# Performance work log

Measured on AMD Instinct MI355X. Metric: run time of the kernel, lower is better.

Reference implementation:

```python
import jax, jax.numpy as jnp
import numpy as np

KS = 3          # kernel_size
DIL = 1         # dilation
PAD = DIL * (KS - 1) // 2
HEAD_DIM = 64
SCALE = HEAD_DIM ** (-0.5)


def _unfold_patches(x):
    """Emulate nn.Unfold(KS, DIL, PAD, 1): x [B,d,H,W] -> [B,d,KS*KS,H,W] (zero-padded)."""
    B, d, H, W = x.shape
    xp = jnp.pad(x, ((0, 0), (0, 0), (PAD, PAD), (PAD, PAD)))
    # small fixed loop over the KS*KS kernel offsets (9 slices), same patch order as Unfold
    patches = [xp[:, :, i * DIL:i * DIL + H, j * DIL:j * DIL + W]
               for i in range(KS) for j in range(KS)]
    return jnp.stack(patches, axis=2)  # [B, d, KS*KS, H, W]


def setup_inputs() -> dict:
    key = jax.random.key(0)
    kq, kk, kv = jax.random.split(key, 3)
    shape = (32, 64, 64, 64)  # [B, head_dim, H, W]
    return {
        "q": jax.random.normal(kq, shape, dtype=jnp.float32),
        "k": jax.random.normal(kk, shape, dtype=jnp.float32),
        "v": jax.random.normal(kv, shape, dtype=jnp.float32),
    }


def reference(q, k, v):
    # q: [B,d,H,W]; per-pixel attention over the KS*KS dilated neighborhood of k/v
    k_p = _unfold_patches(k)                                   # [B,d,n,H,W], n = KS*KS
    attn = jnp.einsum('bdhw,bdnhw->bnhw', q, k_p) * SCALE      # [B,n,H,W]
    attn = jax.nn.softmax(attn, axis=1)                        # softmax over window (dim=-1 in torch layout)
    v_p = _unfold_patches(v)                                   # [B,d,n,H,W]
    out = jnp.einsum('bnhw,bdnhw->bdhw', attn, v_p)            # [B,d,H,W]
    return out
```

## Files before the change

kernel.cpp:

```cpp
#include <hip/hip_runtime.h>

namespace {
constexpr int Bn = 32, Dn = 64, Hn = 64, Wn = 64;
constexpr int PLANE = Hn * Wn;
constexpr int NW  = 4;
constexpr int DPW = Dn / NW;
constexpr float SCALE = 0.125f;
typedef float f4a __attribute__((ext_vector_type(4), aligned(4)));
}

__global__ __launch_bounds__(256, 4) void dilate_attn_kernel(
    const float* __restrict__ q, const float* __restrict__ k,
    const float* __restrict__ v, float* __restrict__ out)
{
    __shared__ float2 red[NW][9][64];

    const int t  = threadIdx.x;
    const int l  = t & 63;
    const int wv = t >> 6;
    const int ci = l & 31;
    const int lr = l >> 5;
    const int c  = ci * 2;

    const int bid = blockIdx.x;
    const int swz = (bid & 7) * 128 + (bid >> 3);
    const int b      = swz >> 5;
    const int stripe = swz & 31;
    const int hr     = stripe * 2 + lr;

    const int  base = b * Dn * PLANE;
    const bool ci0 = (ci == 0), ci31 = (ci == 31);

    const int cb = ci0 ? 0 : (ci31 ? (c - 2) : (c - 1));

    int  koff[3];
    bool rok[3];
#pragma unroll
    for (int di = 0; di < 3; ++di) {
        const int kr = hr - 1 + di;
        rok[di] = (kr >= 0) && (kr < Hn);
        const int krc = min(max(kr, 0), Hn - 1);
        koff[di] = krc * Wn + cb;
    }
    const int qoff = hr * Wn + c;

    float a0[9], a1[9];
#pragma unroll
    for (int n = 0; n < 9; ++n) { a0[n] = 0.0f; a1[n] = 0.0f; }

    {
        const float* kp = k + base + wv * DPW * PLANE;
        const float* qp = q + base + wv * DPW * PLANE;
#pragma unroll 4
        for (int ds = 0; ds < DPW; ++ds) {
            const f4a r0 = *(const f4a*)(kp + koff[0]);
            const f4a r1 = *(const f4a*)(kp + koff[1]);
            const f4a r2 = *(const f4a*)(kp + koff[2]);
            const float2 qv = *(const float2*)(qp + qoff);
            kp += PLANE; qp += PLANE;
#pragma unroll
            for (int di = 0; di < 3; ++di) {
                const f4a vv = (di == 0) ? r0 : (di == 1) ? r1 : r2;
                const float w0 = ci31 ? vv.y : vv.x;
                const float w1 = ci0 ? vv.x : (ci31 ? vv.z : vv.y);
                const float w2 = ci0 ? vv.y : (ci31 ? vv.w : vv.z);
                const float w3 = ci0 ? vv.z : vv.w;
                a0[di * 3 + 0] = fmaf(qv.x, w0, a0[di * 3 + 0]);
                a0[di * 3 + 1] = fmaf(qv.x, w1, a0[di * 3 + 1]);
                a0[di * 3 + 2] = fmaf(qv.x, w2, a0[di * 3 + 2]);
                a1[di * 3 + 0] = fmaf(qv.y, w1, a1[di * 3 + 0]);
                a1[di * 3 + 1] = fmaf(qv.y, w2, a1[di * 3 + 1]);
                a1[di * 3 + 2] = fmaf(qv.y, w3, a1[di * 3 + 2]);
            }
        }
    }

#pragma unroll
    for (int n = 0; n < 9; ++n) red[wv][n][l] = make_float2(a0[n], a1[n]);
    __syncthreads();
#pragma unroll
    for (int n = 0; n < 9; ++n) {
        float2 s = red[0][n][l];
#pragma unroll
        for (int ow = 1; ow < NW; ++ow) {
            const float2 p = red[ow][n][l];
            s.x += p.x; s.y += p.y;
        }
        a0[n] = s.x; a1[n] = s.y;
    }

#pragma unroll
    for (int di = 0; di < 3; ++di)
#pragma unroll
        for (int dj = 0; dj < 3; ++dj) {
            const int n = di * 3 + dj;
            a0[n] = (rok[di] && (dj != 0 || !ci0))  ? a0[n] : 0.0f;
            a1[n] = (rok[di] && (dj != 2 || !ci31)) ? a1[n] : 0.0f;
        }
#pragma unroll
    for (int n = 0; n < 9; ++n) { a0[n] *= SCALE; a1[n] *= SCALE; }
    float m0 = a0[0], m1 = a1[0];
#pragma unroll
    for (int n = 1; n < 9; ++n) { m0 = fmaxf(m0, a0[n]); m1 = fmaxf(m1, a1[n]); }
    float s0 = 0.0f, s1 = 0.0f;
#pragma unroll
    for (int n = 0; n < 9; ++n) {
        a0[n] = __expf(a0[n] - m0); s0 += a0[n];
        a1[n] = __expf(a1[n] - m1); s1 += a1[n];
    }
    const float i0 = 1.0f / s0, i1 = 1.0f / s1;
#pragma unroll
    for (int n = 0; n < 9; ++n) { a0[n] *= i0; a1[n] *= i1; }

#pragma unroll
    for (int di = 0; di < 3; ++di)
#pragma unroll
        for (int dj = 0; dj < 3; ++dj) {
            const int n = di * 3 + dj;
            a0[n] = (rok[di] && (dj != 0 || !ci0))  ? a0[n] : 0.0f;
            a1[n] = (rok[di] && (dj != 2 || !ci31)) ? a1[n] : 0.0f;
        }

    {
        const float* vp = v + base + wv * DPW * PLANE;
        float*       op = out + base + wv * DPW * PLANE;
#pragma unroll 4
        for (int ds = 0; ds < DPW; ++ds) {
            const f4a r0 = *(const f4a*)(vp + koff[0]);
            const f4a r1 = *(const f4a*)(vp + koff[1]);
            const f4a r2 = *(const f4a*)(vp + koff[2]);
            vp += PLANE;
            float o0 = 0.0f, o1 = 0.0f;
#pragma unroll
            for (int di = 0; di < 3; ++di) {
                const f4a vv = (di == 0) ? r0 : (di == 1) ? r1 : r2;
                const float w0 = ci31 ? vv.y : vv.x;
                const float w1 = ci0 ? vv.x : (ci31 ? vv.z : vv.y);
                const float w2 = ci0 ? vv.y : (ci31 ? vv.w : vv.z);
                const float w3 = ci0 ? vv.z : vv.w;
                o0 = fmaf(a0[di * 3 + 0], w0, o0);
                o0 = fmaf(a0[di * 3 + 1], w1, o0);
                o0 = fmaf(a0[di * 3 + 2], w2, o0);
                o1 = fmaf(a1[di * 3 + 0], w1, o1);
                o1 = fmaf(a1[di * 3 + 1], w2, o1);
                o1 = fmaf(a1[di * 3 + 2], w3, o1);
            }
            *(float2*)(op + qoff) = make_float2(o0, o1);
            op += PLANE;
        }
    }
}

extern "C" void kernel_launch(void* const* d_in, const int* in_sizes, int n_in,
                              void* d_out, int out_size, void* d_ws, size_t ws_size,
                              hipStream_t stream) {
    const float* q = (const float*)d_in[0];
    const float* k = (const float*)d_in[1];
    const float* v = (const float*)d_in[2];
    float* out = (float*)d_out;
    (void)in_sizes; (void)n_in; (void)out_size; (void)d_ws; (void)ws_size;

    const int grid = Bn * 32;
    dilate_attn_kernel<<<grid, 256, 0, stream>>>(q, k, v, out);
}
```

Measured before the change: 30.14 us.

## Split head dim across 8 waves, parallelize reduction, double-buffer loads

Raises the number of waves per block from 4 to 8, so each wave handles 8 channels instead of 16, and launches 512 threads per block. The cross-wave reduction is rewritten so each wave sums one window slot in shared memory, with the last wave also summing the ninth slot, and a second barrier is added. The K and V loops are fully unrolled with explicit two-stage register double-buffering to overlap loads with FMAs. The aim is more memory-level parallelism and shorter per-wave serial loops, at the cost of an extra barrier, larger blocks and higher register pressure under the 512,8 launch bounds.

```diff
diff --git a/kernel.cpp b/kernel.cpp
--- a/kernel.cpp
+++ b/kernel.cpp
@@ -3,13 +3,13 @@
 namespace {
 constexpr int Bn = 32, Dn = 64, Hn = 64, Wn = 64;
 constexpr int PLANE = Hn * Wn;
-constexpr int NW  = 4;
+constexpr int NW  = 8;
 constexpr int DPW = Dn / NW;
 constexpr float SCALE = 0.125f;
 typedef float f4a __attribute__((ext_vector_type(4), aligned(4)));
 }
 
-__global__ __launch_bounds__(256, 4) void dilate_attn_kernel(
+__global__ __launch_bounds__(512, 8) void dilate_attn_kernel(
     const float* __restrict__ q, const float* __restrict__ k,
     const float* __restrict__ v, float* __restrict__ out)
 {
@@ -30,8 +30,7 @@
 
     const int  base = b * Dn * PLANE;
     const bool ci0 = (ci == 0), ci31 = (ci == 31);
-
-    const int cb = ci0 ? 0 : (ci31 ? (c - 2) : (c - 1));
+    const int  cb = ci0 ? 0 : (ci31 ? (c - 2) : (c - 1));
 
     int  koff[3];
     bool rok[3];
@@ -50,14 +49,20 @@
 
     {
         const float* kp = k + base + wv * DPW * PLANE;
-        const float* qp = q + base + wv * DPW * PLANE;
-#pragma unroll 4
-        for (int ds = 0; ds < DPW; ++ds) {
-            const f4a r0 = *(const f4a*)(kp + koff[0]);
-            const f4a r1 = *(const f4a*)(kp + koff[1]);
-            const f4a r2 = *(const f4a*)(kp + koff[2]);
-            const float2 qv = *(const float2*)(qp + qoff);
-            kp += PLANE; qp += PLANE;
+        const float* qp = q + base + wv * DPW * PLANE + qoff;
+
+        f4a x0, x1, x2; float2 xq;
+        f4a y0, y1, y2; float2 yq;
+
+        auto LDK = [&](int ds, f4a& r0, f4a& r1, f4a& r2, float2& qv) {
+            const float* kk = kp + ds * PLANE;
+            r0 = *(const f4a*)(kk + koff[0]);
+            r1 = *(const f4a*)(kk + koff[1]);
+            r2 = *(const f4a*)(kk + koff[2]);
+            qv = *(const float2*)(qp + ds * PLANE);
+        };
+        auto ACC = [&](const f4a& r0, const f4a& r1, const f4a& r2,
+                       const float2& qv) {
 #pragma unroll
             for (int di = 0; di < 3; ++di) {
                 const f4a vv = (di == 0) ? r0 : (di == 1) ? r1 : r2;
@@ -72,20 +77,43 @@
                 a1[di * 3 + 1] = fmaf(qv.y, w2, a1[di * 3 + 1]);
                 a1[di * 3 + 2] = fmaf(qv.y, w3, a1[di * 3 + 2]);
             }
+        };
+
+        LDK(0, x0, x1, x2, xq);
+#pragma unroll
+        for (int ds = 0; ds < DPW; ds += 2) {
+            if (ds + 1 < DPW) LDK(ds + 1, y0, y1, y2, yq);
+            ACC(x0, x1, x2, xq);
+            if (ds + 2 < DPW) LDK(ds + 2, x0, x1, x2, xq);
+            if (ds + 1 < DPW) ACC(y0, y1, y2, yq);
         }
     }
 
 #pragma unroll
     for (int n = 0; n < 9; ++n) red[wv][n][l] = make_float2(a0[n], a1[n]);
     __syncthreads();
+    {
+        float2 s = red[0][wv][l];
+#pragma unroll
+        for (int sw = 1; sw < NW; ++sw) {
+            const float2 p = red[sw][wv][l];
+            s.x += p.x; s.y += p.y;
+        }
+        red[0][wv][l] = s;
+        if (wv == NW - 1) {
+            float2 s8 = red[0][8][l];
+#pragma unroll
+            for (int sw = 1; sw < NW; ++sw) {
+                const float2 p = red[sw][8][l];
+                s8.x += p.x; s8.y += p.y;
+            }
+            red[0][8][l] = s8;
+        }
+    }
+    __syncthreads();
 #pragma unroll
     for (int n = 0; n < 9; ++n) {
-        float2 s = red[0][n][l];
-#pragma unroll
-        for (int ow = 1; ow < NW; ++ow) {
-            const float2 p = red[ow][n][l];
-            s.x += p.x; s.y += p.y;
-        }
+        const float2 s = red[0][n][l];
         a0[n] = s.x; a1[n] = s.y;
     }
 
@@ -123,13 +151,18 @@
 
     {
         const float* vp = v + base + wv * DPW * PLANE;
-        float*       op = out + base + wv * DPW * PLANE;
-#pragma unroll 4
-        for (int ds = 0; ds < DPW; ++ds) {
-            const f4a r0 = *(const f4a*)(vp + koff[0]);
-            const f4a r1 = *(const f4a*)(vp + koff[1]);
-            const f4a r2 = *(const f4a*)(vp + koff[2]);
-            vp += PLANE;
+        float*       op = out + base + wv * DPW * PLANE + qoff;
+
+        f4a x0, x1, x2;
+        f4a y0, y1, y2;
+
+        auto LDV = [&](int ds, f4a& r0, f4a& r1, f4a& r2) {
+            const float* vk = vp + ds * PLANE;
+            r0 = *(const f4a*)(vk + koff[0]);
+            r1 = *(const f4a*)(vk + koff[1]);
+            r2 = *(const f4a*)(vk + koff[2]);
+        };
+        auto PV = [&](int ds, const f4a& r0, const f4a& r1, const f4a& r2) {
             float o0 = 0.0f, o1 = 0.0f;
 #pragma unroll
             for (int di = 0; di < 3; ++di) {
@@ -145,8 +178,16 @@
                 o1 = fmaf(a1[di * 3 + 1], w2, o1);
                 o1 = fmaf(a1[di * 3 + 2], w3, o1);
             }
-            *(float2*)(op + qoff) = make_float2(o0, o1);
-            op += PLANE;
+            *(float2*)(op + ds * PLANE) = make_float2(o0, o1);
+        };
+
+        LDV(0, x0, x1, x2);
+#pragma unroll
+        for (int ds = 0; ds < DPW; ds += 2) {
+            if (ds + 1 < DPW) LDV(ds + 1, y0, y1, y2);
+            PV(ds, x0, x1, x2);
+            if (ds + 2 < DPW) LDV(ds + 2, x0, x1, x2);
+            if (ds + 1 < DPW) PV(ds + 1, y0, y1, y2);
         }
     }
 }
@@ -161,5 +202,5 @@
     (void)in_sizes; (void)n_in; (void)out_size; (void)d_ws; (void)ws_size;
 
     const int grid = Bn * 32;
-    dilate_attn_kernel<<<grid, 256, 0, stream>>>(q, k, v, out);
+    dilate_attn_kernel<<<grid, 512, 0, stream>>>(q, k, v, out);
 }
```

After: 67.61 us. 2.24x slower.
